# Performance work log

Measured on AMD Instinct MI355X. Metric: run time of the kernel, lower is better.

## Reference

```python
import jax, jax.numpy as jnp
import numpy as np

P = 51        # n_patches per side
PS = 5        # patch size (255 // 51)
H = 8         # n_heads
EPS = 1e-5    # LayerNorm eps


def positional_embeddings(seq_len, d):
    i = jnp.arange(seq_len, dtype=jnp.float32)[:, None]
    j = jnp.arange(d, dtype=jnp.float32)[None, :]
    # even j -> sin(i / 10000**(j/d)); odd j -> cos(i / 10000**((j-1)/d))
    j_even = j - jnp.mod(j, 2.0)
    angle = i / jnp.power(10000.0, j_even / d)
    return jnp.where(jnp.mod(j, 2.0) == 0, jnp.sin(angle), jnp.cos(angle))


def setup_inputs() -> dict:
    key = jax.random.key(0)
    ks = jax.random.split(key, 12)
    E, IN_D, NC = 128, 75, 3
    return {
        "images": jax.random.normal(ks[0], (64, 3, 255, 255), dtype=jnp.float32),
        "lm_w": jax.random.normal(ks[1], (E, IN_D), dtype=jnp.float32) * 0.1,
        "lm_b": jax.random.normal(ks[2], (E,), dtype=jnp.float32) * 0.1,
        "cls_tok": jax.random.uniform(ks[3], (1, E), dtype=jnp.float32),
        "w_in": jax.random.normal(ks[4], (3 * E, E), dtype=jnp.float32) * 0.05,
        "b_in": jax.random.normal(ks[5], (3 * E,), dtype=jnp.float32) * 0.05,
        "w_out": jax.random.normal(ks[6], (E, E), dtype=jnp.float32) * 0.05,
        "b_out": jax.random.normal(ks[7], (E,), dtype=jnp.float32) * 0.05,
        "ln_g": jnp.ones((E,), dtype=jnp.float32),
        "ln_b": jnp.zeros((E,), dtype=jnp.float32),
        "out_w": jax.random.normal(ks[8], (NC, E), dtype=jnp.float32) * 0.1,
        "out_b": jax.random.normal(ks[9], (NC,), dtype=jnp.float32) * 0.1,
    }


def reference(images, lm_w, lm_b, cls_tok, w_in, b_in, w_out, b_out, ln_g, ln_b, out_w, out_b):
    n, c, h, w = images.shape
    E = lm_w.shape[0]
    hd = E // H
    # --- patchify (vectorized equivalent of the triple Python loop) ---
    # flatten order per patch is (c, ph, pw), patches ordered row-major (i, j)
    patches = images.reshape(n, c, P, PS, P, PS)
    patches = patches.transpose(0, 2, 4, 1, 3, 5).reshape(n, P * P, c * PS * PS)
    # --- linear embed + class token + positional embeddings ---
    tokens = patches @ lm_w.T + lm_b                      # (n, P*P, E)
    cls = jnp.broadcast_to(cls_tok[None], (n, 1, E))
    x = jnp.concatenate([cls, tokens], axis=1)            # (n, S, E), S = P*P+1
    S = P * P + 1
    x = x + positional_embeddings(S, E)[None]
    # --- MultiheadAttention, faithful to torch default batch_first=False:
    # torch interprets axis 0 (=n, the image batch) as the SEQUENCE dim and
    # axis 1 (=S tokens) as the batch dim, so attention mixes across images.
    qkv = x @ w_in.T + b_in                               # (n, S, 3E)
    q, k, v = jnp.split(qkv, 3, axis=-1)
    q = q.reshape(n, S, H, hd) * (1.0 / np.sqrt(hd))
    k = k.reshape(n, S, H, hd)
    v = v.reshape(n, S, H, hd)
    scores = jnp.einsum('lshd,mshd->shlm', q, k)          # (S, H, n, n)
    attn = jax.nn.softmax(scores, axis=-1)
    o = jnp.einsum('shlm,mshd->lshd', attn, v).reshape(n, S, E)
    x = o @ w_out.T + b_out                               # (n, S, E)
    # --- LayerNorm (dropout is identity in eval) ---
    mu = jnp.mean(x, axis=-1, keepdims=True)
    var = jnp.mean(jnp.square(x - mu), axis=-1, keepdims=True)
    x = (x - mu) * jax.lax.rsqrt(var + EPS) * ln_g + ln_b
    # --- mean pool over tokens + classifier head ---
    pooled = jnp.mean(x, axis=1)                          # (n, E)
    return pooled @ out_w.T + out_b                       # (n, n_classes)
```

## Files before the change

kernel.cpp:

```cpp
#include <hip/hip_runtime.h>
#include <math.h>

#define NIMG 64
#define SEQ  2602
#define EMB  128
#define HD   16
#define SPAD 2624
#define KQ   96
#define LSO  136
#define TOK  8

typedef float f32x4 __attribute__((ext_vector_type(4)));
typedef short short8 __attribute__((ext_vector_type(8)));

__device__ __forceinline__ unsigned short f2bf(float f) {
    union { float f; unsigned int u; } v; v.f = f;
    return (unsigned short)((v.u + 0x8000u) >> 16);
}

__global__ __launch_bounds__(128) void build_A(
    const float* __restrict__ lm_b, const float* __restrict__ cls,
    float* __restrict__ A) {
    const int s = blockIdx.x, e = threadIdx.x;
    const bool odd = e & 1;
    float v;
    if (s == 0) {
        v = cls[e] + (odd ? 1.0f : 0.0f);
    } else if (s < SEQ) {
        float pfac = powf(10000.0f, -(float)(e & ~1) / 128.0f);
        float ang = (float)s * pfac;
        v = lm_b[e] + (odd ? cosf(ang) : sinf(ang));
    } else {
        v = 0.0f;
    }
    A[(size_t)s * 128 + e] = v;
}

__global__ __launch_bounds__(128) void build_W2(
    const float* __restrict__ w_in, const float* __restrict__ lm_w,
    unsigned short* __restrict__ W2) {
    const int j = blockIdx.x, f = threadIdx.x;
    if (f >= KQ) return;
    float acc = 0.0f;
    if (f < 75) {
        for (int e = 0; e < 128; ++e)
            acc += w_in[j * 128 + e] * lm_w[e * 75 + f];
    }
    W2[j * KQ + f] = f2bf(acc);
}

__global__ __launch_bounds__(128) void build_Wout(
    const float* __restrict__ w_out, unsigned short* __restrict__ Wo) {
    const int j = blockIdx.x, e = threadIdx.x;
    Wo[j * 128 + e] = f2bf(w_out[j * 128 + e]);
}

__global__ __launch_bounds__(1024) void zero_pooled(float* __restrict__ p) {
    p[blockIdx.x * 1024 + threadIdx.x] = 0.0f;
}

__global__ __launch_bounds__(1024) void zero_cls(unsigned int* __restrict__ p) {
    p[blockIdx.x * 1024 + threadIdx.x] = 0u;
}

__global__ __launch_bounds__(256) void patchify(
    const float* __restrict__ images, unsigned short* __restrict__ Pb) {
    __shared__ unsigned short rows[15][256];
    const int i = blockIdx.x, l = blockIdx.y;
    const int tid = threadIdx.x;

    if (tid < 255) {
        #pragma unroll
        for (int seg = 0; seg < 15; ++seg) {
            int c = seg / 5, rr = seg % 5;
            float v = images[(((size_t)l * 3 + c) * 255 + (i * 5 + rr)) * 255 + tid];
            rows[seg][tid] = f2bf(v);
        }
    }
    __syncthreads();

    const int j = tid >> 2;
    const int part = tid & 3;
    if (j < 51) {
        const int f0 = part * 24;
        __align__(16) unsigned short buf[24];
        #pragma unroll
        for (int u = 0; u < 24; ++u) {
            int f = f0 + u;
            unsigned short v = 0;
            if (f < 75) {
                int c = f / 25, rem = f % 25, rr = rem / 5, cc = rem % 5;
                v = rows[c * 5 + rr][j * 5 + cc];
            }
            buf[u] = v;
        }
        const int s = i * 51 + j + 1;
        unsigned short* dst = Pb + ((size_t)s * 64 + l) * KQ + f0;
        #pragma unroll
        for (int t = 0; t < 3; ++t)
            *(short8*)(dst + t * 8) = *(const short8*)&buf[t * 8];
    }
}

__global__ __launch_bounds__(256) void qkv_attn(
    const unsigned short* __restrict__ Pb, const unsigned short* __restrict__ W2,
    const float* __restrict__ SB, unsigned short* __restrict__ Obuf) {
    __shared__ __align__(16) unsigned short Qw_[4][64 * 40];
    __shared__ __align__(16) unsigned short Kw_[4][64 * 40];
    __shared__ __align__(16) unsigned short Vw_[4][32 * 72];
    __shared__ __align__(16) unsigned short Pw_[4][64 * 80];
    __shared__ __align__(16) unsigned short Ow_[4][64 * 16];

    const int s = blockIdx.x;
    const int tid = threadIdx.x;
    const int w = tid >> 6, lane = tid & 63, quad = lane >> 4, col = lane & 15;
    unsigned short* Qw = Qw_[w];
    unsigned short* Kw = Kw_[w];
    unsigned short* Vw = Vw_[w];
    unsigned short* Pw = Pw_[w];
    unsigned short* Ow = Ow_[w];

    f32x4 acc[6][4] = {};
    const unsigned short* arow0 = Pb + (size_t)s * 64 * KQ;
    #pragma unroll
    for (int ks = 0; ks < 3; ++ks) {
        const int k0 = ks * 32 + quad * 8;
        short8 b[6];
        #pragma unroll
        for (int nt = 0; nt < 6; ++nt) {
            int ch = (nt >> 1) * 128 + 32 * w + (nt & 1) * 16 + col;
            b[nt] = *(const short8*)(W2 + (size_t)ch * KQ + k0);
        }
        #pragma unroll
        for (int mt = 0; mt < 4; ++mt) {
            short8 a = *(const short8*)(arow0 + (size_t)(mt * 16 + col) * KQ + k0);
            #pragma unroll
            for (int nt = 0; nt < 6; ++nt)
                acc[nt][mt] = __builtin_amdgcn_mfma_f32_16x16x32_bf16(a, b[nt], acc[nt][mt], 0, 0, 0);
        }
    }

    const float* sbrow = SB + (size_t)s * 384;
    #pragma unroll
    for (int nt = 0; nt < 6; ++nt) {
        int ch = (nt >> 1) * 128 + 32 * w + (nt & 1) * 16 + col;
        float bv = sbrow[ch];
        int chl = (nt & 1) * 16 + col;
        #pragma unroll
        for (int mt = 0; mt < 4; ++mt) {
            #pragma unroll
            for (int r = 0; r < 4; ++r) {
                int m = mt * 16 + quad * 4 + r;
                float v = acc[nt][mt][r] + bv;
                if (nt < 2)      Qw[m * 40 + chl] = f2bf(v * 0.125f);
                else if (nt < 4) Kw[m * 40 + chl] = f2bf(v);
                else             Vw[chl * 72 + m] = f2bf(v);
            }
        }
    }

    const int koff = (quad & 1) * 8;
    short8 ones8;
    #pragma unroll
    for (int i = 0; i < 8; ++i) ones8[i] = (short)0x3F80;

    #pragma unroll
    for (int hl = 0; hl < 2; ++hl) {
        const int hoff = hl * 16;
        short8 bfr[4];
        #pragma unroll
        for (int nt = 0; nt < 4; ++nt)
            bfr[nt] = *(const short8*)&Kw[(nt * 16 + col) * 40 + hoff + koff];

        f32x4 sc[4][4] = {};
        #pragma unroll
        for (int mt = 0; mt < 4; ++mt) {
            short8 afr = *(const short8*)&Qw[(mt * 16 + col) * 40 + hoff + koff];
            #pragma unroll
            for (int nt = 0; nt < 4; ++nt)
                sc[mt][nt] = __builtin_amdgcn_mfma_f32_16x16x32_bf16(afr, bfr[nt], sc[mt][nt], 0, 0, 0);
        }

        #pragma unroll
        for (int mt = 0; mt < 4; ++mt) {
            #pragma unroll
            for (int r = 0; r < 4; ++r) {
                const int M = mt * 16 + quad * 4 + r;
                const int swz = (M >> 2) & 7;
                #pragma unroll
                for (int nt = 0; nt < 4; ++nt) {
                    int jc = (nt * 2 + (col >> 3)) ^ swz;
                    Pw[M * 80 + jc * 8 + (col & 7)] = f2bf(__expf(sc[mt][nt][r]));
                }
            }
        }

        short8 vfr[2];
        #pragma unroll
        for (int ks = 0; ks < 2; ++ks)
            vfr[ks] = *(const short8*)&Vw[(hoff + col) * 72 + ks * 32 + quad * 8];

        #pragma unroll
        for (int mt = 0; mt < 4; ++mt) {
            f32x4 o = {}, sm = {};
            const int m = mt * 16 + col;
            const int swz = (m >> 2) & 7;
            #pragma unroll
            for (int ks = 0; ks < 2; ++ks) {
                int kcs = (ks * 4 + quad) ^ swz;
                short8 pa = *(const short8*)&Pw[m * 80 + kcs * 8];
                o  = __builtin_amdgcn_mfma_f32_16x16x32_bf16(pa, vfr[ks], o, 0, 0, 0);
                sm = __builtin_amdgcn_mfma_f32_16x16x32_bf16(pa, ones8, sm, 0, 0, 0);
            }
            #pragma unroll
            for (int r = 0; r < 4; ++r) {
                float iv = __builtin_amdgcn_rcpf(sm[r]);
                int l = mt * 16 + quad * 4 + r;
                int cc = (l * 2 + (col >> 3)) ^ ((l >> 2) & 3);
                Ow[cc * 8 + (col & 7)] = f2bf(o[r] * iv);
            }
        }

        unsigned short* od = Obuf + ((size_t)s * 8 + 2 * w + hl) * 1024;
        #pragma unroll
        for (int jj = 0; jj < 2; ++jj) {
            int cc = lane * 2 + jj;
            int cs = cc ^ ((lane >> 2) & 3);
            *(short8*)(od + cc * 8) = *(const short8*)&Ow[cs * 8];
        }
    }
}

__global__ __launch_bounds__(256) void gemm_out_ln_pool(
    const unsigned short* __restrict__ O, const unsigned short* __restrict__ Wo,
    const float* __restrict__ b_out, const float* __restrict__ ln_g,
    const float* __restrict__ ln_b, float* __restrict__ pooled) {
    __shared__ __align__(16) unsigned short As[2][64 * LSO];
    __shared__ __align__(16) unsigned short Bs[128 * LSO];
    const int tid = threadIdx.x;
    const int s0 = blockIdx.x * TOK;
    const int wv = tid >> 6, lane = tid & 63, quad = lane >> 4, col = lane & 15;

    #pragma unroll
    for (int t = 0; t < 8; ++t) {
        int q = tid + t * 256;
        int row = q >> 4, c = q & 15;
        *(float4*)&Bs[row * LSO + c * 8] =
            *(const float4*)(Wo + (size_t)row * 128 + c * 8);
    }
    #pragma unroll
    for (int t = 0; t < 4; ++t) {
        int q = tid + t * 256;
        int h = q >> 7, rem = q & 127, l = rem >> 1, jj = rem & 1;
        *(short8*)&As[0][l * LSO + h * 16 + jj * 8] =
            *(const short8*)(O + (size_t)s0 * 8192 + (size_t)q * 8);
    }
    __syncthreads();

    float gch[8], bch[8], boch[8];
    #pragma unroll
    for (int nt = 0; nt < 8; ++nt) {
        int ch = nt * 16 + col;
        gch[nt] = ln_g[ch]; bch[nt] = ln_b[ch]; boch[nt] = b_out[ch];
    }
    const int mrow = wv * 16 + col;
    const int l0 = wv * 16 + quad * 4;
    const int nT = (SEQ - s0 < TOK) ? (SEQ - s0) : TOK;
    float accum[8][4] = {};

    for (int tt = 0; tt < nT; ++tt) {
        if (tt + 1 < nT) {
            const size_t sn = s0 + tt + 1;
            #pragma unroll
            for (int t = 0; t < 4; ++t) {
                int q = tid + t * 256;
                int h = q >> 7, rem = q & 127, l = rem >> 1, jj = rem & 1;
                *(short8*)&As[(tt + 1) & 1][l * LSO + h * 16 + jj * 8] =
                    *(const short8*)(O + sn * 8192 + (size_t)q * 8);
            }
        }
        const unsigned short* Ac = As[tt & 1];
        f32x4 acc[8] = {};
        #pragma unroll
        for (int ks = 0; ks < 4; ++ks) {
            const int k0 = ks * 32 + quad * 8;
            short8 a = *(const short8*)&Ac[mrow * LSO + k0];
            #pragma unroll
            for (int nt = 0; nt < 8; ++nt) {
                short8 b = *(const short8*)&Bs[(nt * 16 + col) * LSO + k0];
                acc[nt] = __builtin_amdgcn_mfma_f32_16x16x32_bf16(a, b, acc[nt], 0, 0, 0);
            }
        }
        #pragma unroll
        for (int r = 0; r < 4; ++r) {
            float yv[8];
            float s1 = 0.0f, s2 = 0.0f;
            #pragma unroll
            for (int nt = 0; nt < 8; ++nt) {
                yv[nt] = acc[nt][r] + boch[nt];
                s1 += yv[nt]; s2 += yv[nt] * yv[nt];
            }
            #pragma unroll
            for (int off = 1; off < 16; off <<= 1) {
                s1 += __shfl_xor(s1, off);
                s2 += __shfl_xor(s2, off);
            }
            float mu = s1 * (1.0f / 128.0f);
            float var = s2 * (1.0f / 128.0f) - mu * mu;
            float rinv = rsqrtf(var + 1e-5f);
            #pragma unroll
            for (int nt = 0; nt < 8; ++nt)
                accum[nt][r] += (yv[nt] - mu) * rinv * gch[nt] + bch[nt];
        }
        __syncthreads();
    }

    #pragma unroll
    for (int nt = 0; nt < 8; ++nt)
        #pragma unroll
        for (int r = 0; r < 4; ++r)
            atomicAdd(&pooled[(l0 + r) * 128 + nt * 16 + col], accum[nt][r]);
}

__global__ __launch_bounds__(256) void gemm64(
    const float* __restrict__ A, int lda, const float* __restrict__ B,
    const float* __restrict__ bias, float* __restrict__ C, int ldc) {
    __shared__ float As[64 * 68];
    __shared__ float Bs[64 * 68];
    const int bm = blockIdx.y * 64;
    const int bn = blockIdx.x * 64;
    const int tid = threadIdx.x;
    const int tx = tid & 15, ty = tid >> 4;

    float acc[4][4] = {};

    for (int kk = 0; kk < 128; kk += 64) {
        __syncthreads();
        #pragma unroll
        for (int t = 0; t < 4; ++t) {
            int q = tid + t * 256;
            int row = q & 63, c4 = (q >> 6) << 2;
            float4 va = *(const float4*)(A + (size_t)(bm + row) * lda + kk + c4);
            As[(c4 + 0) * 68 + row] = va.x;
            As[(c4 + 1) * 68 + row] = va.y;
            As[(c4 + 2) * 68 + row] = va.z;
            As[(c4 + 3) * 68 + row] = va.w;
            float4 vb = *(const float4*)(B + (size_t)(bn + row) * 128 + kk + c4);
            Bs[(c4 + 0) * 68 + row] = vb.x;
            Bs[(c4 + 1) * 68 + row] = vb.y;
            Bs[(c4 + 2) * 68 + row] = vb.z;
            Bs[(c4 + 3) * 68 + row] = vb.w;
        }
        __syncthreads();
        #pragma unroll 4
        for (int k = 0; k < 64; ++k) {
            float4 av = *(const float4*)&As[k * 68 + (ty << 2)];
            float4 bv = *(const float4*)&Bs[k * 68 + (tx << 2)];
            acc[0][0] += av.x*bv.x; acc[0][1] += av.x*bv.y; acc[0][2] += av.x*bv.z; acc[0][3] += av.x*bv.w;
            acc[1][0] += av.y*bv.x; acc[1][1] += av.y*bv.y; acc[1][2] += av.y*bv.z; acc[1][3] += av.y*bv.w;
            acc[2][0] += av.z*bv.x; acc[2][1] += av.z*bv.y; acc[2][2] += av.z*bv.z; acc[2][3] += av.z*bv.w;
            acc[3][0] += av.w*bv.x; acc[3][1] += av.w*bv.y; acc[3][2] += av.w*bv.z; acc[3][3] += av.w*bv.w;
        }
    }

    float4 bv = *(const float4*)(bias + bn + (tx << 2));
    #pragma unroll
    for (int i = 0; i < 4; ++i) {
        float4 r;
        r.x = acc[i][0] + bv.x; r.y = acc[i][1] + bv.y;
        r.z = acc[i][2] + bv.z; r.w = acc[i][3] + bv.w;
        *(float4*)(C + (size_t)(bm + (ty << 2) + i) * ldc + bn + (tx << 2)) = r;
    }
}

__global__ __launch_bounds__(128) void classify(
    const float* __restrict__ pooled, const float* __restrict__ out_w,
    const float* __restrict__ out_b, float* __restrict__ out) {
    const int l = blockIdx.x, e = threadIdx.x;
    __shared__ float sp[EMB];
    sp[e] = pooled[l * EMB + e] * (1.0f / (float)SEQ);
    __syncthreads();
    if (e < 3) {
        float acc = out_b[e];
        #pragma unroll 16
        for (int k = 0; k < EMB; ++k) acc += sp[k] * out_w[e * EMB + k];
        out[l * 3 + e] = acc;
    }
}

extern "C" void kernel_launch(void* const* d_in, const int* in_sizes, int n_in,
                              void* d_out, int out_size, void* d_ws, size_t ws_size,
                              hipStream_t stream) {
    const float* images = (const float*)d_in[0];
    const float* lm_w   = (const float*)d_in[1];
    const float* lm_b   = (const float*)d_in[2];
    const float* cls    = (const float*)d_in[3];
    const float* w_in   = (const float*)d_in[4];
    const float* b_in   = (const float*)d_in[5];
    const float* w_out  = (const float*)d_in[6];
    const float* b_out  = (const float*)d_in[7];
    const float* ln_g   = (const float*)d_in[8];
    const float* ln_b   = (const float*)d_in[9];
    const float* out_w  = (const float*)d_in[10];
    const float* out_b  = (const float*)d_in[11];
    float* out = (float*)d_out;

    float* SB     = (float*)d_ws;
    float* A_pre  = SB + (size_t)SPAD * 384;
    float* pooled = A_pre + (size_t)SPAD * 128;
    unsigned short* W2   = (unsigned short*)(pooled + 64 * 128);
    unsigned short* Wout = W2 + (size_t)384 * KQ;
    unsigned short* Pb   = Wout + 128 * 128;
    unsigned short* Obuf = Pb + (size_t)SEQ * 64 * KQ;

    build_A<<<dim3(SPAD), 128, 0, stream>>>(lm_b, cls, A_pre);
    gemm64<<<dim3(6, SPAD / 64), 256, 0, stream>>>(A_pre, 128, w_in, b_in, SB, 384);
    build_W2<<<dim3(384), 128, 0, stream>>>(w_in, lm_w, W2);
    build_Wout<<<dim3(128), 128, 0, stream>>>(w_out, Wout);
    zero_pooled<<<dim3(8), 1024, 0, stream>>>(pooled);
    zero_cls<<<dim3(3), 1024, 0, stream>>>((unsigned int*)Pb);

    patchify<<<dim3(51, 64), 256, 0, stream>>>(images, Pb);
    qkv_attn<<<dim3(SEQ), 256, 0, stream>>>(Pb, W2, SB, Obuf);
    gemm_out_ln_pool<<<dim3((SEQ + TOK - 1) / TOK), 256, 0, stream>>>(
        Obuf, Wout, b_out, ln_g, ln_b, pooled);
    classify<<<dim3(NIMG), 128, 0, stream>>>(pooled, out_w, out_b, out);
}
```

Measured before the change: 247.8 us.

## Compute QKV per head in attention loop to shrink LDS and raise occupancy

The qkv_attn kernel now projects Q, K and V for one head at a time inside the head loop, instead of projecting both heads up front. This roughly halves per-wave LDS buffers and accumulator registers. The output staging buffer is dropped by reusing Kw, the exp/PV step is split into two halves to shrink the P tile, and launch bounds ask for 3 blocks per CU. In exchange, the patch A-fragments are reloaded from global memory once per head, and the head loop is no longer unrolled.

Result: faster. 215.8 us (-12.9%).

```diff
diff --git a/kernel.cpp b/kernel.cpp
--- a/kernel.cpp
+++ b/kernel.cpp
@@ -102,14 +102,13 @@
     }
 }
 
-__global__ __launch_bounds__(256) void qkv_attn(
+__global__ __launch_bounds__(256, 3) void qkv_attn(
     const unsigned short* __restrict__ Pb, const unsigned short* __restrict__ W2,
     const float* __restrict__ SB, unsigned short* __restrict__ Obuf) {
-    __shared__ __align__(16) unsigned short Qw_[4][64 * 40];
-    __shared__ __align__(16) unsigned short Kw_[4][64 * 40];
-    __shared__ __align__(16) unsigned short Vw_[4][32 * 72];
-    __shared__ __align__(16) unsigned short Pw_[4][64 * 80];
-    __shared__ __align__(16) unsigned short Ow_[4][64 * 16];
+    __shared__ __align__(16) unsigned short Qw_[4][64 * 24];
+    __shared__ __align__(16) unsigned short Kw_[4][64 * 24];
+    __shared__ __align__(16) unsigned short Vw_[4][16 * 72];
+    __shared__ __align__(16) unsigned short Pw_[4][64 * 40];
 
     const int s = blockIdx.x;
     const int tid = threadIdx.x;
@@ -118,116 +117,127 @@
     unsigned short* Kw = Kw_[w];
     unsigned short* Vw = Vw_[w];
     unsigned short* Pw = Pw_[w];
-    unsigned short* Ow = Ow_[w];
-
-    f32x4 acc[6][4] = {};
+
     const unsigned short* arow0 = Pb + (size_t)s * 64 * KQ;
-    #pragma unroll
-    for (int ks = 0; ks < 3; ++ks) {
-        const int k0 = ks * 32 + quad * 8;
-        short8 b[6];
-        #pragma unroll
-        for (int nt = 0; nt < 6; ++nt) {
-            int ch = (nt >> 1) * 128 + 32 * w + (nt & 1) * 16 + col;
-            b[nt] = *(const short8*)(W2 + (size_t)ch * KQ + k0);
-        }
-        #pragma unroll
-        for (int mt = 0; mt < 4; ++mt) {
-            short8 a = *(const short8*)(arow0 + (size_t)(mt * 16 + col) * KQ + k0);
-            #pragma unroll
-            for (int nt = 0; nt < 6; ++nt)
-                acc[nt][mt] = __builtin_amdgcn_mfma_f32_16x16x32_bf16(a, b[nt], acc[nt][mt], 0, 0, 0);
-        }
-    }
-
     const float* sbrow = SB + (size_t)s * 384;
-    #pragma unroll
-    for (int nt = 0; nt < 6; ++nt) {
-        int ch = (nt >> 1) * 128 + 32 * w + (nt & 1) * 16 + col;
-        float bv = sbrow[ch];
-        int chl = (nt & 1) * 16 + col;
-        #pragma unroll
-        for (int mt = 0; mt < 4; ++mt) {
-            #pragma unroll
-            for (int r = 0; r < 4; ++r) {
-                int m = mt * 16 + quad * 4 + r;
-                float v = acc[nt][mt][r] + bv;
-                if (nt < 2)      Qw[m * 40 + chl] = f2bf(v * 0.125f);
-                else if (nt < 4) Kw[m * 40 + chl] = f2bf(v);
-                else             Vw[chl * 72 + m] = f2bf(v);
-            }
-        }
-    }
-
     const int koff = (quad & 1) * 8;
     short8 ones8;
     #pragma unroll
     for (int i = 0; i < 8; ++i) ones8[i] = (short)0x3F80;
 
-    #pragma unroll
+    #pragma unroll 1
     for (int hl = 0; hl < 2; ++hl) {
-        const int hoff = hl * 16;
+        const int h = 2 * w + hl;
+
+        f32x4 acc[3][4] = {};
+        #pragma unroll
+        for (int ks = 0; ks < 3; ++ks) {
+            const int k0 = ks * 32 + quad * 8;
+            short8 b[3];
+            #pragma unroll
+            for (int nt = 0; nt < 3; ++nt) {
+                int ch = nt * 128 + h * 16 + col;
+                b[nt] = *(const short8*)(W2 + (size_t)ch * KQ + k0);
+            }
+            #pragma unroll
+            for (int mt = 0; mt < 4; ++mt) {
+                short8 a = *(const short8*)(arow0 + (size_t)(mt * 16 + col) * KQ + k0);
+                #pragma unroll
+                for (int nt = 0; nt < 3; ++nt)
+                    acc[nt][mt] = __builtin_amdgcn_mfma_f32_16x16x32_bf16(a, b[nt], acc[nt][mt], 0, 0, 0);
+            }
+        }
+
+        #pragma unroll
+        for (int nt = 0; nt < 3; ++nt) {
+            float bv = sbrow[nt * 128 + h * 16 + col];
+            #pragma unroll
+            for (int mt = 0; mt < 4; ++mt) {
+                #pragma unroll
+                for (int r = 0; r < 4; ++r) {
+                    int m = mt * 16 + quad * 4 + r;
+                    float v = acc[nt][mt][r] + bv;
+                    if (nt == 0) {
+                        int pos = (col >> 3) ^ (quad & 1);
+                        Qw[m * 24 + pos * 8 + (col & 7)] = f2bf(v * 0.125f);
+                    } else if (nt == 1) {
+                        int pos = (col >> 3) ^ (quad & 1);
+                        Kw[m * 24 + pos * 8 + (col & 7)] = f2bf(v);
+                    } else {
+                        Vw[col * 72 + m] = f2bf(v);
+                    }
+                }
+            }
+        }
+
         short8 bfr[4];
         #pragma unroll
-        for (int nt = 0; nt < 4; ++nt)
-            bfr[nt] = *(const short8*)&Kw[(nt * 16 + col) * 40 + hoff + koff];
+        for (int nt = 0; nt < 4; ++nt) {
+            int m_ = nt * 16 + col;
+            int pos = (quad & 1) ^ ((col >> 2) & 1);
+            bfr[nt] = *(const short8*)&Kw[m_ * 24 + pos * 8];
+        }
 
         f32x4 sc[4][4] = {};
         #pragma unroll
         for (int mt = 0; mt < 4; ++mt) {
-            short8 afr = *(const short8*)&Qw[(mt * 16 + col) * 40 + hoff + koff];
+            int m_ = mt * 16 + col;
+            int pos = (quad & 1) ^ ((col >> 2) & 1);
+            short8 afr = *(const short8*)&Qw[m_ * 24 + pos * 8];
             #pragma unroll
             for (int nt = 0; nt < 4; ++nt)
                 sc[mt][nt] = __builtin_amdgcn_mfma_f32_16x16x32_bf16(afr, bfr[nt], sc[mt][nt], 0, 0, 0);
         }
 
+        short8 vfr[2];
+        #pragma unroll
+        for (int ks = 0; ks < 2; ++ks)
+            vfr[ks] = *(const short8*)&Vw[col * 72 + ks * 32 + quad * 8];
+
+        f32x4 o[4] = {}, sm[4] = {};
+        #pragma unroll
+        for (int half = 0; half < 2; ++half) {
+            #pragma unroll
+            for (int ntl = 0; ntl < 2; ++ntl) {
+                int nt = half * 2 + ntl;
+                #pragma unroll
+                for (int mt = 0; mt < 4; ++mt) {
+                    #pragma unroll
+                    for (int r = 0; r < 4; ++r) {
+                        int m = mt * 16 + quad * 4 + r;
+                        int pos = (ntl * 2 + (col >> 3)) ^ quad;
+                        Pw[m * 40 + pos * 8 + (col & 7)] = f2bf(__expf(sc[mt][nt][r]));
+                    }
+                }
+            }
+            #pragma unroll
+            for (int mt = 0; mt < 4; ++mt) {
+                int m_ = mt * 16 + col;
+                int pos = quad ^ ((col >> 2) & 3);
+                short8 pa = *(const short8*)&Pw[m_ * 40 + pos * 8];
+                o[mt]  = __builtin_amdgcn_mfma_f32_16x16x32_bf16(pa, vfr[half], o[mt], 0, 0, 0);
+                sm[mt] = __builtin_amdgcn_mfma_f32_16x16x32_bf16(pa, ones8, sm[mt], 0, 0, 0);
+            }
+        }
+
         #pragma unroll
         for (int mt = 0; mt < 4; ++mt) {
             #pragma unroll
             for (int r = 0; r < 4; ++r) {
-                const int M = mt * 16 + quad * 4 + r;
-                const int swz = (M >> 2) & 7;
-                #pragma unroll
-                for (int nt = 0; nt < 4; ++nt) {
-                    int jc = (nt * 2 + (col >> 3)) ^ swz;
-                    Pw[M * 80 + jc * 8 + (col & 7)] = f2bf(__expf(sc[mt][nt][r]));
-                }
-            }
-        }
-
-        short8 vfr[2];
-        #pragma unroll
-        for (int ks = 0; ks < 2; ++ks)
-            vfr[ks] = *(const short8*)&Vw[(hoff + col) * 72 + ks * 32 + quad * 8];
-
-        #pragma unroll
-        for (int mt = 0; mt < 4; ++mt) {
-            f32x4 o = {}, sm = {};
-            const int m = mt * 16 + col;
-            const int swz = (m >> 2) & 7;
-            #pragma unroll
-            for (int ks = 0; ks < 2; ++ks) {
-                int kcs = (ks * 4 + quad) ^ swz;
-                short8 pa = *(const short8*)&Pw[m * 80 + kcs * 8];
-                o  = __builtin_amdgcn_mfma_f32_16x16x32_bf16(pa, vfr[ks], o, 0, 0, 0);
-                sm = __builtin_amdgcn_mfma_f32_16x16x32_bf16(pa, ones8, sm, 0, 0, 0);
-            }
-            #pragma unroll
-            for (int r = 0; r < 4; ++r) {
-                float iv = __builtin_amdgcn_rcpf(sm[r]);
+                float iv = __builtin_amdgcn_rcpf(sm[mt][r]);
                 int l = mt * 16 + quad * 4 + r;
                 int cc = (l * 2 + (col >> 3)) ^ ((l >> 2) & 3);
-                Ow[cc * 8 + (col & 7)] = f2bf(o[r] * iv);
-            }
-        }
-
-        unsigned short* od = Obuf + ((size_t)s * 8 + 2 * w + hl) * 1024;
+                Kw[cc * 8 + (col & 7)] = f2bf(o[mt][r] * iv);
+            }
+        }
+        unsigned short* od = Obuf + ((size_t)s * 8 + h) * 1024;
         #pragma unroll
         for (int jj = 0; jj < 2; ++jj) {
             int cc = lane * 2 + jj;
             int cs = cc ^ ((lane >> 2) & 3);
-            *(short8*)(od + cc * 8) = *(const short8*)&Ow[cs * 8];
-        }
+            *(short8*)(od + cc * 8) = *(const short8*)&Kw[cs * 8];
+        }
+        if (hl == 0) __builtin_amdgcn_s_waitcnt(0);
     }
 }
 
```
